# Kernel optimization log

Hardware: AMD Instinct MI355X
Metric: run time of the kernel (lower is better)

## Reference

```python
import jax, jax.numpy as jnp
import numpy as np

B, H, W, C = 8, 112, 112, 128
NH, WS, SR, HIDDEN = 4, 7, 8, 512
EPS = 1e-5

def ln(x, g, b):
    mu = jnp.mean(x, axis=-1, keepdims=True)
    var = jnp.var(x, axis=-1, keepdims=True)
    return (x - mu) * jax.lax.rsqrt(var + EPS) * g + b

def local_attn(x, qkv_w, qkv_b, pw, pb):
    # windowed attention: (H,W) tiled into WSxWS windows, H%WS==W%WS==0 so no pad
    Bx, N, Cx = x.shape
    hd = Cx // NH
    _h, _w = H // WS, W // WS
    xw = x.reshape(Bx, _h, WS, _w, WS, Cx).transpose(0, 1, 3, 2, 4, 5)
    xw = xw.reshape(Bx, _h * _w, WS * WS, Cx)
    qkv = (xw @ qkv_w + qkv_b).reshape(Bx, _h * _w, WS * WS, 3, NH, hd)
    qkv = qkv.transpose(3, 0, 1, 4, 2, 5)  # 3, B, nW, NH, ws2, hd
    q, k, v = qkv[0], qkv[1], qkv[2]
    attn = jax.nn.softmax((q @ jnp.swapaxes(k, -2, -1)) * (hd ** -0.5), axis=-1)
    o = (attn @ v).transpose(0, 1, 3, 2, 4).reshape(Bx, _h, _w, WS, WS, Cx)
    o = o.transpose(0, 1, 3, 2, 4, 5).reshape(Bx, N, Cx)
    return o @ pw + pb

def global_attn(x, qw, qb, kvw, kvb, srw, srb, sng, snb, pw, pb):
    Bx, N, Cx = x.shape
    hd = Cx // NH
    q = (x @ qw + qb).reshape(Bx, N, NH, hd).transpose(0, 2, 1, 3)  # B,NH,N,hd
    xi = x.reshape(Bx, H, W, Cx)
    xs = jax.lax.conv_general_dilated(xi, srw, (SR, SR), 'VALID',
                                      dimension_numbers=('NHWC', 'HWIO', 'NHWC')) + srb
    xs = ln(xs.reshape(Bx, -1, Cx), sng, snb)  # B, M, C  (M = (H/SR)*(W/SR))
    kv = (xs @ kvw + kvb).reshape(Bx, -1, 2, NH, hd)
    k = kv[:, :, 0].transpose(0, 2, 1, 3)
    v = kv[:, :, 1].transpose(0, 2, 1, 3)
    attn = jax.nn.softmax(jnp.einsum('bhnd,bhmd->bhnm', q, k) * (hd ** -0.5), axis=-1)
    o = jnp.einsum('bhnm,bhmd->bhnd', attn, v).transpose(0, 2, 1, 3).reshape(Bx, N, Cx)
    return o @ pw + pb

def mlp(x, f1w, f1b, dww, dwb, f2w, f2b):
    h = x @ f1w + f1b
    hi = h.reshape(x.shape[0], H, W, HIDDEN)
    hi = jax.lax.conv_general_dilated(hi, dww, (1, 1), 'SAME',
                                      dimension_numbers=('NHWC', 'HWIO', 'NHWC'),
                                      feature_group_count=HIDDEN) + dwb
    h = jax.nn.gelu(hi.reshape(x.shape[0], -1, HIDDEN), approximate=False)
    return h @ f2w + f2b

def reference(x, l_n1_g, l_n1_b, l_qkv_w, l_qkv_b, l_pw, l_pb, l_n2_g, l_n2_b,
              l_f1w, l_f1b, l_dww, l_dwb, l_f2w, l_f2b,
              g_n1_g, g_n1_b, g_qw, g_qb, g_kvw, g_kvb, g_srw, g_srb, g_sng, g_snb,
              g_pw, g_pb, g_n2_g, g_n2_b, g_f1w, g_f1b, g_dww, g_dwb, g_f2w, g_f2b):
    # Local-attention Block
    x = x + local_attn(ln(x, l_n1_g, l_n1_b), l_qkv_w, l_qkv_b, l_pw, l_pb)
    x = x + mlp(ln(x, l_n2_g, l_n2_b), l_f1w, l_f1b, l_dww, l_dwb, l_f2w, l_f2b)
    # Global (spatial-reduction) attention Block
    x = x + global_attn(ln(x, g_n1_g, g_n1_b), g_qw, g_qb, g_kvw, g_kvb,
                        g_srw, g_srb, g_sng, g_snb, g_pw, g_pb)
    x = x + mlp(ln(x, g_n2_g, g_n2_b), g_f1w, g_f1b, g_dww, g_dwb, g_f2w, g_f2b)
    return x

def setup_inputs() -> dict:
    key = jax.random.key(0)
    cnt = [0]
    def rn(shp, s=0.02):
        cnt[0] += 1
        return (jax.random.normal(jax.random.fold_in(key, cnt[0]), shp, dtype=jnp.float32) * s)
    z = lambda shp: jnp.zeros(shp, jnp.float32)
    o = lambda shp: jnp.ones(shp, jnp.float32)
    return {
        'x': rn((B, H * W, C), 1.0),
        'l_n1_g': o((C,)), 'l_n1_b': z((C,)),
        'l_qkv_w': rn((C, 3 * C)), 'l_qkv_b': z((3 * C,)),
        'l_pw': rn((C, C)), 'l_pb': z((C,)),
        'l_n2_g': o((C,)), 'l_n2_b': z((C,)),
        'l_f1w': rn((C, HIDDEN)), 'l_f1b': z((HIDDEN,)),
        'l_dww': rn((3, 3, 1, HIDDEN), 0.1), 'l_dwb': z((HIDDEN,)),
        'l_f2w': rn((HIDDEN, C)), 'l_f2b': z((C,)),
        'g_n1_g': o((C,)), 'g_n1_b': z((C,)),
        'g_qw': rn((C, C)), 'g_qb': z((C,)),
        'g_kvw': rn((C, 2 * C)), 'g_kvb': z((2 * C,)),
        'g_srw': rn((SR, SR, C, C), 0.02), 'g_srb': z((C,)),
        'g_sng': o((C,)), 'g_snb': z((C,)),
        'g_pw': rn((C, C)), 'g_pb': z((C,)),
        'g_n2_g': o((C,)), 'g_n2_b': z((C,)),
        'g_f1w': rn((C, HIDDEN)), 'g_f1b': z((HIDDEN,)),
        'g_dww': rn((3, 3, 1, HIDDEN), 0.1), 'g_dwb': z((HIDDEN,)),
        'g_f2w': rn((HIDDEN, C)), 'g_f2b': z((C,)),
    }
```

## Files before the change

### kernel.cpp

```cpp
#include <hip/hip_runtime.h>
#include <hip/hip_bf16.h>

#define DI __device__ __forceinline__

typedef __attribute__((ext_vector_type(8))) __bf16 bf16x8;
typedef __attribute__((ext_vector_type(8))) short short8;
typedef __attribute__((ext_vector_type(4))) short short4v;
typedef __attribute__((ext_vector_type(4))) float f32x4;

DI short f2b(float f) {
    union { float f; unsigned u; } v; v.f = f;
    unsigned r = v.u + 0x7FFFu + ((v.u >> 16) & 1u);
    return (short)(r >> 16);
}
DI float b2f(short s) {
    union { unsigned u; float f; } v; v.u = ((unsigned)(unsigned short)s) << 16;
    return v.f;
}
DI float lo16(int x) {
    union { unsigned u; float f; } v; v.u = (unsigned)x << 16; return v.f;
}
DI float hi16(int x) {
    union { unsigned u; float f; } v; v.u = (unsigned)x & 0xffff0000u; return v.f;
}

DI void gll16(const short* g, short* l) {
    __builtin_amdgcn_global_load_lds(
        (const __attribute__((address_space(1))) void*)(g),
        (__attribute__((address_space(3))) void*)(l), 16, 0, 0);
}

DI float gelu(float a) {
    float z = fabsf(a) * 0.7071067811865475f;
    float t = __builtin_amdgcn_rcpf(fmaf(0.3275911f, z, 1.f));
    float p = t * fmaf(t, fmaf(t, fmaf(t, fmaf(t, 1.061405429f, -1.453152027f),
                                       1.421413741f), -0.284496736f), 0.254829592f);
    float e = __expf(-z * z);
    float er = fmaf(-p, e, 1.f);
    float sg = (a >= 0.f) ? er : -er;
    return 0.5f * a * (1.f + sg);
}

template<int OB, int HB, int HR, int LNO>
__global__ __launch_bounds__(512)
void gemm128(const short* __restrict__ A, int lda,
             const short* __restrict__ Wt, int ldw,
             const float* __restrict__ bias,
             void* __restrict__ Cv, int ldc,
             const short* __restrict__ R, int ldr,
             const float* __restrict__ lng, const float* __restrict__ lnb,
             short* __restrict__ lnout,
             int K)
{
    __shared__ short As[8192];
    __shared__ short Bs[8192];
    const int nx = gridDim.x;
    const int total = nx * gridDim.y;
    int bid = blockIdx.x + nx * blockIdx.y;
    if ((total & 7) == 0) bid = (bid & 7) * (total >> 3) + (bid >> 3);
    const int m0 = (bid / nx) * 128, n0 = (bid % nx) * 128;
    const int tid = threadIdx.x, lane = tid & 63, w = tid >> 6;
    const int wr = w >> 2, wc = w & 3;
    const int fr = lane & 15, fg = lane >> 4;
    const int mB = wr * 64 + fr;
    const int nB = wc * 32 + fg * 4;

    const int r0 = tid >> 2, p0 = tid & 3;
    const int s0 = (r0 & 3) ^ ((r0 >> 2) & 3);
    const short* aptr0 = A + (long long)(m0 + r0) * lda + (p0 ^ s0) * 8;
    const short* bptr0 = Wt + (long long)(n0 + r0) * ldw + (p0 ^ s0) * 8;

    const int sf = (fr & 3) ^ ((fr >> 2) & 3);
    const short* pA = As + (wr * 64 + fr) * 32 + (fg ^ sf) * 8;
    const short* pB = Bs + (wc * 32 + fr) * 32 + (fg ^ sf) * 8;

    int2 rpre[4][2];
    if (HR) {
        #pragma unroll
        for (int mi = 0; mi < 4; mi++) {
            const long long m = m0 + mB + mi * 16;
            #pragma unroll
            for (int ni = 0; ni < 2; ni++)
                rpre[mi][ni] = *(const int2*)&R[m * ldr + n0 + nB + ni * 16];
        }
    }

    f32x4 zero = {0.f, 0.f, 0.f, 0.f};
    f32x4 acc[4][2];
    #pragma unroll
    for (int i = 0; i < 4; i++)
        #pragma unroll
        for (int j = 0; j < 2; j++) acc[i][j] = zero;

    auto STAGE = [&](int buf, int t) {
        const int o = t * 32;
        gll16(aptr0 + o, As + buf * 4096 + w * 512);
        gll16(bptr0 + o, Bs + buf * 4096 + w * 512);
    };
    auto COMPUTE = [&](int buf) {
        const short* qA = pA + buf * 4096;
        const short* qB = pB + buf * 4096;
        bf16x8 af[4], bfr[2];
        #pragma unroll
        for (int i = 0; i < 4; i++) af[i] = *(const bf16x8*)(qA + i * 512);
        #pragma unroll
        for (int j = 0; j < 2; j++) bfr[j] = *(const bf16x8*)(qB + j * 512);
        __builtin_amdgcn_s_setprio(1);
        #pragma unroll
        for (int i = 0; i < 4; i++)
            #pragma unroll
            for (int j = 0; j < 2; j++)
                acc[i][j] = __builtin_amdgcn_mfma_f32_16x16x32_bf16(bfr[j], af[i], acc[i][j], 0, 0, 0);
        __builtin_amdgcn_s_setprio(0);
    };

    const int NT = K >> 5;
    STAGE(0, 0);
    for (int t = 0; t < NT; t++) {
        if (t + 1 < NT) {
            STAGE((t + 1) & 1, t + 1);
            asm volatile("s_waitcnt vmcnt(2)" ::: "memory");
        } else {
            asm volatile("s_waitcnt vmcnt(0)" ::: "memory");
        }
        __builtin_amdgcn_s_barrier();
        COMPUTE(t & 1);
        __builtin_amdgcn_s_barrier();
    }

    if (LNO) {
        float s1[4] = {0.f, 0.f, 0.f, 0.f}, s2[4] = {0.f, 0.f, 0.f, 0.f};
        #pragma unroll
        for (int mi = 0; mi < 4; mi++) {
            const long long m = m0 + mB + mi * 16;
            #pragma unroll
            for (int ni = 0; ni < 2; ni++) {
                const int n = nB + ni * 16;
                float4 bv = *(const float4*)&bias[n];
                const float* bvp = (const float*)&bv;
                float rv[4] = {lo16(rpre[mi][ni].x), hi16(rpre[mi][ni].x),
                               lo16(rpre[mi][ni].y), hi16(rpre[mi][ni].y)};
                #pragma unroll
                for (int v = 0; v < 4; v++) {
                    float val = acc[mi][ni][v] + bvp[v] + rv[v];
                    acc[mi][ni][v] = val;
                    s1[mi] += val;
                    s2[mi] += val * val;
                }
                int2 pk;
                pk.x = ((int)(unsigned short)f2b(acc[mi][ni][1]) << 16) | (unsigned short)f2b(acc[mi][ni][0]);
                pk.y = ((int)(unsigned short)f2b(acc[mi][ni][3]) << 16) | (unsigned short)f2b(acc[mi][ni][2]);
                *(int2*)&((short*)Cv)[m * ldc + n] = pk;
            }
        }
        #pragma unroll
        for (int mi = 0; mi < 4; mi++) {
            s1[mi] += __shfl_xor(s1[mi], 16); s1[mi] += __shfl_xor(s1[mi], 32);
            s2[mi] += __shfl_xor(s2[mi], 16); s2[mi] += __shfl_xor(s2[mi], 32);
        }
        float* sc = (float*)As;
        __syncthreads();
        if (fg == 0) {
            #pragma unroll
            for (int mi = 0; mi < 4; mi++) {
                int rt = mB + mi * 16;
                sc[rt * 8 + wc * 2]     = s1[mi];
                sc[rt * 8 + wc * 2 + 1] = s2[mi];
            }
        }
        __syncthreads();
        #pragma unroll
        for (int mi = 0; mi < 4; mi++) {
            int rt = mB + mi * 16;
            long long m = m0 + rt;
            float t1 = (sc[rt * 8 + 0] + sc[rt * 8 + 2]) + (sc[rt * 8 + 4] + sc[rt * 8 + 6]);
            float t2 = (sc[rt * 8 + 1] + sc[rt * 8 + 3]) + (sc[rt * 8 + 5] + sc[rt * 8 + 7]);
            float mu = t1 * 0.0078125f;
            float var = t2 * 0.0078125f - mu * mu;
            float rs = rsqrtf(var + 1e-5f);
            #pragma unroll
            for (int ni = 0; ni < 2; ni++) {
                int n = nB + ni * 16;
                float4 gg = *(const float4*)&lng[n];
                float4 bb = *(const float4*)&lnb[n];
                const float* gp = (const float*)&gg;
                const float* bp = (const float*)&bb;
                short o[4];
                #pragma unroll
                for (int v = 0; v < 4; v++)
                    o[v] = f2b((acc[mi][ni][v] - mu) * rs * gp[v] + bp[v]);
                int2 pk;
                pk.x = ((int)(unsigned short)o[1] << 16) | (unsigned short)o[0];
                pk.y = ((int)(unsigned short)o[3] << 16) | (unsigned short)o[2];
                *(int2*)&lnout[m * 128 + n] = pk;
            }
        }
    } else {
        #pragma unroll
        for (int mi = 0; mi < 4; mi++) {
            const long long m = m0 + mB + mi * 16;
            #pragma unroll
            for (int ni = 0; ni < 2; ni++) {
                const int n = n0 + nB + ni * 16;
                float4 bv = {0.f, 0.f, 0.f, 0.f};
                if (HB) bv = *(const float4*)&bias[n];
                const float* bvp = (const float*)&bv;
                float rv[4] = {0.f, 0.f, 0.f, 0.f};
                if (HR) {
                    rv[0] = lo16(rpre[mi][ni].x); rv[1] = hi16(rpre[mi][ni].x);
                    rv[2] = lo16(rpre[mi][ni].y); rv[3] = hi16(rpre[mi][ni].y);
                }
                float val[4];
                #pragma unroll
                for (int v = 0; v < 4; v++)
                    val[v] = acc[mi][ni][v] + bvp[v] + rv[v];
                if (OB) {
                    int2 pk;
                    pk.x = ((int)(unsigned short)f2b(val[1]) << 16) | (unsigned short)f2b(val[0]);
                    pk.y = ((int)(unsigned short)f2b(val[3]) << 16) | (unsigned short)f2b(val[2]);
                    *(int2*)&((short*)Cv)[m * ldc + n] = pk;
                } else {
                    float4 st = {val[0], val[1], val[2], val[3]};
                    *(float4*)&((float*)Cv)[m * ldc + n] = st;
                }
            }
        }
    }
}

template<int OB, int HB>
__global__ __launch_bounds__(256)
void gemm64(const short* __restrict__ A, int lda, long long sA,
            const short* __restrict__ Wt, int ldw, long long sW,
            const float* __restrict__ bias,
            void* __restrict__ Cv, int ldc, long long sC,
            int M, int N, int K)
{
    __shared__ short As[2048];
    __shared__ short Bs[2048];
    const int z = blockIdx.z;
    A  += (long long)z * sA;
    Wt += (long long)z * sW;
    const int m0 = blockIdx.y * 64, n0 = blockIdx.x * 64;
    const int tid = threadIdx.x, lane = tid & 63, wv = tid >> 6;
    const int wr = wv >> 1, wc = wv & 1;
    const int lrow = tid >> 2, lch = tid & 3;
    const int wch = lch ^ (lrow & 3);

    f32x4 zero = {0.f, 0.f, 0.f, 0.f};
    f32x4 acc00 = zero, acc01 = zero, acc10 = zero, acc11 = zero;

    const short* arow = &A[(long long)(m0 + lrow) * lda + lch * 8];
    const short* brow = &Wt[(long long)(n0 + lrow) * ldw + lch * 8];
    short* asw = &As[lrow * 32 + wch * 8];
    short* bsw = &Bs[lrow * 32 + wch * 8];

    const int fr = lane & 15, fg = lane >> 4;
    const int c = ((fg ^ (fr & 3)) * 8);
    const int a0off = (wr * 32 + fr) * 32 + c;
    const int b0off = (wc * 32 + fr) * 32 + c;

    for (int k0 = 0; k0 < K; k0 += 32) {
        uint4 av = *(const uint4*)arow; arow += 32;
        uint4 bv = *(const uint4*)brow; brow += 32;
        __syncthreads();
        *(uint4*)asw = av;
        *(uint4*)bsw = bv;
        __syncthreads();
        bf16x8 a0 = *(const bf16x8*)&As[a0off];
        bf16x8 a1 = *(const bf16x8*)&As[a0off + 512];
        bf16x8 b0 = *(const bf16x8*)&Bs[b0off];
        bf16x8 b1 = *(const bf16x8*)&Bs[b0off + 512];
        acc00 = __builtin_amdgcn_mfma_f32_16x16x32_bf16(a0, b0, acc00, 0, 0, 0);
        acc01 = __builtin_amdgcn_mfma_f32_16x16x32_bf16(a0, b1, acc01, 0, 0, 0);
        acc10 = __builtin_amdgcn_mfma_f32_16x16x32_bf16(a1, b0, acc10, 0, 0, 0);
        acc11 = __builtin_amdgcn_mfma_f32_16x16x32_bf16(a1, b1, acc11, 0, 0, 0);
    }

    const long long cz = (long long)z * sC;
    const int rbase = m0 + wr * 32 + fg * 4;
    const int cbase = n0 + wc * 32 + fr;
    auto emit = [&](f32x4 a, int mi, int ni) {
        int cc = cbase + ni * 16;
        if (cc >= N) return;
        float bv = HB ? bias[cc] : 0.f;
        #pragma unroll
        for (int v = 0; v < 4; v++) {
            int rr = rbase + mi * 16 + v;
            if (rr >= M) continue;
            float val = a[v] + bv;
            if (OB) ((short*)Cv)[cz + (long long)rr * ldc + cc] = f2b(val);
            else    ((float*)Cv)[cz + (long long)rr * ldc + cc] = val;
        }
    };
    emit(acc00, 0, 0); emit(acc01, 0, 1); emit(acc10, 1, 0); emit(acc11, 1, 1);
}

__global__ __launch_bounds__(256)
void srgemm(const short* __restrict__ LNF, const short* __restrict__ Wt,
            float* __restrict__ PART)
{
    __shared__ short As[2048];
    __shared__ short Bs[2048];
    const int z = blockIdx.z;
    const int m0 = blockIdx.y * 64, n0 = blockIdx.x * 64;
    const int tid = threadIdx.x, lane = tid & 63, wv = tid >> 6;
    const int wr = wv >> 1, wc = wv & 1;
    const int lrow = tid >> 2, lch = tid & 3;
    const int wch = lch ^ (lrow & 3);

    f32x4 zero = {0.f, 0.f, 0.f, 0.f};
    f32x4 acc00 = zero, acc01 = zero, acc10 = zero, acc11 = zero;

    int row = m0 + lrow;
    int rc = row < 1568 ? row : 1567;
    int b = rc / 196, p = rc % 196;
    int oh = p / 14, ow = p % 14;
    int k0 = z * 256;
    int kh = k0 >> 10, koff = k0 & 1023;
    const short* arow = LNF + ((long long)(b * 12544 + (oh * 8 + kh) * 112 + ow * 8)) * 128
                        + koff + lch * 8;
    const short* brow = Wt + (long long)(n0 + lrow) * 8192 + k0 + lch * 8;
    short* asw = &As[lrow * 32 + wch * 8];
    short* bsw = &Bs[lrow * 32 + wch * 8];

    const int fr = lane & 15, fg = lane >> 4;
    const int c = ((fg ^ (fr & 3)) * 8);
    const int a0off = (wr * 32 + fr) * 32 + c;
    const int b0off = (wc * 32 + fr) * 32 + c;

    for (int kk = 0; kk < 256; kk += 32) {
        uint4 av = *(const uint4*)arow; arow += 32;
        uint4 bv = *(const uint4*)brow; brow += 32;
        __syncthreads();
        *(uint4*)asw = av;
        *(uint4*)bsw = bv;
        __syncthreads();
        bf16x8 a0 = *(const bf16x8*)&As[a0off];
        bf16x8 a1 = *(const bf16x8*)&As[a0off + 512];
        bf16x8 b0 = *(const bf16x8*)&Bs[b0off];
        bf16x8 b1 = *(const bf16x8*)&Bs[b0off + 512];
        acc00 = __builtin_amdgcn_mfma_f32_16x16x32_bf16(a0, b0, acc00, 0, 0, 0);
        acc01 = __builtin_amdgcn_mfma_f32_16x16x32_bf16(a0, b1, acc01, 0, 0, 0);
        acc10 = __builtin_amdgcn_mfma_f32_16x16x32_bf16(a1, b0, acc10, 0, 0, 0);
        acc11 = __builtin_amdgcn_mfma_f32_16x16x32_bf16(a1, b1, acc11, 0, 0, 0);
    }

    const int rbase = m0 + wr * 32 + fg * 4;
    const int cbase = n0 + wc * 32 + fr;
    auto emit = [&](f32x4 a, int mi, int ni) {
        int cc = cbase + ni * 16;
        #pragma unroll
        for (int v = 0; v < 4; v++) {
            int rr = rbase + mi * 16 + v;
            if (rr >= 1568) continue;
            PART[(long long)z * 200704 + (long long)rr * 128 + cc] = a[v];
        }
    };
    emit(acc00, 0, 0); emit(acc01, 0, 1); emit(acc10, 1, 0); emit(acc11, 1, 1);
}

__global__ void reduceXS(const float* __restrict__ PART, const float* __restrict__ bias,
                         float* __restrict__ XS)
{
    int i = blockIdx.x * 256 + threadIdx.x;
    float s = 0.f;
    #pragma unroll
    for (int z = 0; z < 32; z++) s += PART[(long long)z * 200704 + i];
    XS[i] = s + bias[i & 127];
}

__global__ __launch_bounds__(256)
void ln_kernel(const float* __restrict__ x, const float* __restrict__ g,
               const float* __restrict__ b, short* __restrict__ o, int rows)
{
    int row = blockIdx.x * 4 + (threadIdx.x >> 6);
    if (row >= rows) return;
    int lane = threadIdx.x & 63;
    const float2 v = *(const float2*)&x[(long long)row * 128 + lane * 2];
    float s = v.x + v.y;
    float ss = v.x * v.x + v.y * v.y;
    #pragma unroll
    for (int off = 1; off < 64; off <<= 1) {
        s += __shfl_xor(s, off);
        ss += __shfl_xor(ss, off);
    }
    float mu = s * 0.0078125f;
    float var = ss * 0.0078125f - mu * mu;
    float rs = rsqrtf(var + 1e-5f);
    float2 gg = *(const float2*)&g[lane * 2];
    float2 bb = *(const float2*)&b[lane * 2];
    short2 out;
    out.x = f2b((v.x - mu) * rs * gg.x + bb.x);
    out.y = f2b((v.y - mu) * rs * gg.y + bb.y);
    *(short2*)&o[(long long)row * 128 + lane * 2] = out;
}

__global__ __launch_bounds__(256)
void ln_first(const float* __restrict__ x, const float* __restrict__ g,
              const float* __restrict__ b, short* __restrict__ o,
              short* __restrict__ res)
{
    int row = blockIdx.x * 4 + (threadIdx.x >> 6);
    int lane = threadIdx.x & 63;
    const float2 v = *(const float2*)&x[(long long)row * 128 + lane * 2];
    short2 rc;
    rc.x = f2b(v.x); rc.y = f2b(v.y);
    *(short2*)&res[(long long)row * 128 + lane * 2] = rc;
    float s = v.x + v.y;
    float ss = v.x * v.x + v.y * v.y;
    #pragma unroll
    for (int off = 1; off < 64; off <<= 1) {
        s += __shfl_xor(s, off);
        ss += __shfl_xor(ss, off);
    }
    float mu = s * 0.0078125f;
    float var = ss * 0.0078125f - mu * mu;
    float rs = rsqrtf(var + 1e-5f);
    float2 gg = *(const float2*)&g[lane * 2];
    float2 bb = *(const float2*)&b[lane * 2];
    short2 out;
    out.x = f2b((v.x - mu) * rs * gg.x + bb.x);
    out.y = f2b((v.y - mu) * rs * gg.y + bb.y);
    *(short2*)&o[(long long)row * 128 + lane * 2] = out;
}

__global__ void wtrans(const float* __restrict__ w, short* __restrict__ wt, int K, int N)
{
    long long idx = (long long)blockIdx.x * 256 + threadIdx.x;
    if (idx >= (long long)K * N) return;
    int k = (int)(idx / N), n = (int)(idx % N);
    wt[(long long)n * K + k] = f2b(w[idx]);
}

__global__ void packkv(const short* __restrict__ kvb, short* __restrict__ kp,
                       short* __restrict__ vt)
{
    int idx = blockIdx.x * 256 + threadIdx.x;
    if (idx >= 229376) return;
    int d = idx & 31;
    int m = (idx >> 5) % 224;
    int bh = idx / (224 * 32);
    int b = bh >> 2, h = bh & 3;
    short kv = 0, vv = 0;
    if (m < 196) {
        long long src = ((long long)b * 196 + m) * 256 + h * 32 + d;
        kv = kvb[src];
        vv = kvb[src + 128];
    }
    if (m < 208) kp[((long long)bh * 208 + m) * 32 + d] = kv;
    vt[((long long)bh * 32 + d) * 224 + m] = vv;
}

__global__ __launch_bounds__(512)
void lattn(const short* __restrict__ qkv, short* __restrict__ att)
{
    __shared__ short QKs[64 * 264];
    __shared__ short Vt[128 * 72];
    __shared__ short Pl[8 * 16 * 72];
    const int bi = blockIdx.x >> 8;
    const int win = blockIdx.x & 255;
    const int wy = win >> 4, wx = win & 15;
    const long long base = (long long)bi * 12544;
    const int tid = threadIdx.x;

    for (int i = tid; i < 1152; i += 512) {
        uint4 zz = {0, 0, 0, 0};
        *(uint4*)&Vt[i * 8] = zz;
    }
    __syncthreads();

    for (int idx = tid; idx < 2352; idx += 512) {
        int i = idx / 48, ch = idx % 48;
        long long n = base + (wy * 7 + i / 7) * 112 + wx * 7 + i % 7;
        uint4 v = *(const uint4*)&qkv[n * 384 + ch * 8];
        if (ch < 32) {
            *(uint4*)&QKs[i * 264 + ch * 8] = v;
        } else {
            int c0 = (ch - 32) * 8;
            const short* sp = (const short*)&v;
            #pragma unroll
            for (int u = 0; u < 8; u++) {
                int cc = c0 + u;
                Vt[cc * 72 + ((((i >> 3) ^ ((cc >> 3) & 7)) << 3) | (i & 7))] = sp[u];
            }
        }
    }
    __syncthreads();

    const int w = tid >> 6, l = tid & 63;
    const int h = w >> 1, qh = w & 1;
    const int q16 = l & 15, g = l >> 4;
    const float SC = 0.17677669529663689f;
    f32x4 zero = {0.f, 0.f, 0.f, 0.f};

    bf16x8 kf[4];
    #pragma unroll
    for (int kt = 0; kt < 4; kt++)
        kf[kt] = *(const bf16x8*)&QKs[(kt * 16 + q16) * 264 + 128 + h * 32 + g * 8];
    bf16x8 vf[2][2];
    #pragma unroll
    for (int dt = 0; dt < 2; dt++) {
        int cc = h * 32 + dt * 16 + q16;
        #pragma unroll
        for (int s2 = 0; s2 < 2; s2++)
            vf[dt][s2] = *(const bf16x8*)&Vt[cc * 72 + (((s2 * 4 + g) ^ ((cc >> 3) & 7)) << 3)];
    }
    short* pw = &Pl[(w * 16 + q16) * 72];

    for (int qt2 = 0; qt2 < 2; qt2++) {
        int qt = qh * 2 + qt2;
        bf16x8 qf = *(const bf16x8*)&QKs[(qt * 16 + q16) * 264 + h * 32 + g * 8];
        f32x4 s[4];
        #pragma unroll
        for (int kt = 0; kt < 4; kt++)
            s[kt] = __builtin_amdgcn_mfma_f32_16x16x32_bf16(kf[kt], qf, zero, 0, 0, 0);
        float mx = -1e30f;
        #pragma unroll
        for (int kt = 0; kt < 4; kt++) {
            #pragma unroll
            for (int v = 0; v < 4; v++) {
                int k = kt * 16 + g * 4 + v;
                if (k < 49) mx = fmaxf(mx, s[kt][v]);
            }
        }
        mx = fmaxf(mx, __shfl_xor(mx, 16));
        mx = fmaxf(mx, __shfl_xor(mx, 32));
        float sum = 0.f;
        #pragma unroll
        for (int kt = 0; kt < 4; kt++) {
            #pragma unroll
            for (int v = 0; v < 4; v++) {
                int k = kt * 16 + g * 4 + v;
                float p = (k < 49) ? __expf(SC * (s[kt][v] - mx)) : 0.f;
                s[kt][v] = p;
                sum += p;
            }
        }
        sum += __shfl_xor(sum, 16);
        sum += __shfl_xor(sum, 32);
        float inv = 1.f / sum;
        #pragma unroll
        for (int kt = 0; kt < 4; kt++) {
            int lo = ((int)(unsigned short)f2b(s[kt][1] * inv) << 16) | (unsigned short)f2b(s[kt][0] * inv);
            int hi = ((int)(unsigned short)f2b(s[kt][3] * inv) << 16) | (unsigned short)f2b(s[kt][2] * inv);
            int2 pr; pr.x = lo; pr.y = hi;
            *(int2*)&pw[kt * 16 + g * 4] = pr;
        }
        f32x4 o0 = zero, o1 = zero;
        #pragma unroll
        for (int s2 = 0; s2 < 2; s2++) {
            bf16x8 pa = *(const bf16x8*)&pw[s2 * 32 + g * 8];
            o0 = __builtin_amdgcn_mfma_f32_16x16x32_bf16(pa, vf[0][s2], o0, 0, 0, 0);
            o1 = __builtin_amdgcn_mfma_f32_16x16x32_bf16(pa, vf[1][s2], o1, 0, 0, 0);
        }
        #pragma unroll
        for (int v = 0; v < 4; v++) {
            int q = qt * 16 + g * 4 + v;
            if (q < 49) {
                long long n = base + (wy * 7 + q / 7) * 112 + wx * 7 + q % 7;
                att[n * 128 + h * 32 + q16]      = f2b(o0[v]);
                att[n * 128 + h * 32 + 16 + q16] = f2b(o1[v]);
            }
        }
    }
}

__global__ __launch_bounds__(256)
void gattn(const short* __restrict__ Q, const short* __restrict__ KP,
           const short* __restrict__ VT, short* __restrict__ O)
{
    __shared__ short Ks[208 * 40];
    __shared__ short Vt[32 * 232];
    __shared__ short Pl[4 * 16 * 232];
    const int qb = blockIdx.x;
    const int bh = blockIdx.y;
    const int b = bh >> 2, h = bh & 3;
    const int tid = threadIdx.x, w = tid >> 6, l = tid & 63;
    const int q16 = l & 15, g = l >> 4;

    for (int idx = tid; idx < 832; idx += 256) {
        int m = idx >> 2, dg = idx & 3;
        uint4 v = *(const uint4*)&KP[((long long)bh * 208 + m) * 32 + dg * 8];
        *(uint4*)&Ks[m * 40 + ((dg ^ (m & 3)) * 8)] = v;
    }
    for (int idx = tid; idx < 896; idx += 256) {
        int d = idx / 28, mg = idx % 28;
        uint4 v = *(const uint4*)&VT[((long long)bh * 32 + d) * 224 + mg * 8];
        *(uint4*)&Vt[d * 232 + mg * 8] = v;
    }
    const long long qbase = (long long)b * 12544 + qb * 128 + w * 32;
    bf16x8 qfa = *(const bf16x8*)&Q[(qbase + q16) * 128 + h * 32 + g * 8];
    bf16x8 qfb = *(const bf16x8*)&Q[(qbase + 16 + q16) * 128 + h * 32 + g * 8];
    __syncthreads();

    const float SC = 0.17677669529663689f;
    f32x4 zero = {0.f, 0.f, 0.f, 0.f};
    short* pw = &Pl[(w * 16 + q16) * 232];
    const int xk = (g ^ (q16 & 3)) * 8;

    #pragma unroll
    for (int qt = 0; qt < 2; qt++) {
        bf16x8 qf = qt ? qfb : qfa;
        f32x4 s[13];
        #pragma unroll
        for (int t = 0; t < 13; t++) {
            bf16x8 a = *(const bf16x8*)&Ks[(t * 16 + q16) * 40 + xk];
            s[t] = __builtin_amdgcn_mfma_f32_16x16x32_bf16(a, qf, zero, 0, 0, 0);
        }
        float mx = -1e30f;
        #pragma unroll
        for (int t = 0; t < 13; t++) {
            #pragma unroll
            for (int v = 0; v < 4; v++) {
                int k = t * 16 + g * 4 + v;
                if (k < 196) mx = fmaxf(mx, s[t][v]);
            }
        }
        mx = fmaxf(mx, __shfl_xor(mx, 16));
        mx = fmaxf(mx, __shfl_xor(mx, 32));
        float sum = 0.f;
        #pragma unroll
        for (int t = 0; t < 13; t++) {
            #pragma unroll
            for (int v = 0; v < 4; v++) {
                int k = t * 16 + g * 4 + v;
                float pv = (k < 196) ? __expf(SC * (s[t][v] - mx)) : 0.f;
                s[t][v] = pv;
                sum += pv;
            }
        }
        sum += __shfl_xor(sum, 16);
        sum += __shfl_xor(sum, 32);
        float inv = 1.f / sum;
        #pragma unroll
        for (int t = 0; t < 13; t++) {
            int lo = ((int)(unsigned short)f2b(s[t][1] * inv) << 16) | (unsigned short)f2b(s[t][0] * inv);
            int hi = ((int)(unsigned short)f2b(s[t][3] * inv) << 16) | (unsigned short)f2b(s[t][2] * inv);
            int2 pr; pr.x = lo; pr.y = hi;
            *(int2*)&pw[t * 16 + g * 4] = pr;
        }
        int2 zz; zz.x = 0; zz.y = 0;
        *(int2*)&pw[208 + g * 4] = zz;

        f32x4 o0 = zero, o1 = zero;
        #pragma unroll
        for (int kc = 0; kc < 7; kc++) {
            bf16x8 pa = *(const bf16x8*)&pw[kc * 32 + g * 8];
            bf16x8 v0 = *(const bf16x8*)&Vt[q16 * 232 + kc * 32 + g * 8];
            bf16x8 v1 = *(const bf16x8*)&Vt[(16 + q16) * 232 + kc * 32 + g * 8];
            o0 = __builtin_amdgcn_mfma_f32_16x16x32_bf16(v0, pa, o0, 0, 0, 0);
            o1 = __builtin_amdgcn_mfma_f32_16x16x32_bf16(v1, pa, o1, 0, 0, 0);
        }
        const long long r = qbase + qt * 16 + q16;
        int2 p0, p1;
        p0.x = ((int)(unsigned short)f2b(o0[1]) << 16) | (unsigned short)f2b(o0[0]);
        p0.y = ((int)(unsigned short)f2b(o0[3]) << 16) | (unsigned short)f2b(o0[2]);
        p1.x = ((int)(unsigned short)f2b(o1[1]) << 16) | (unsigned short)f2b(o1[0]);
        p1.y = ((int)(unsigned short)f2b(o1[3]) << 16) | (unsigned short)f2b(o1[2]);
        *(int2*)&O[r * 128 + h * 32 + g * 4]      = p0;
        *(int2*)&O[r * 128 + h * 32 + 16 + g * 4] = p1;
    }
}

__global__ __launch_bounds__(256)
void dwgelu(const short* __restrict__ h1, const float* __restrict__ w,
            const float* __restrict__ bias, short* __restrict__ h2)
{
    int bid = blockIdx.x;
    bid = (bid & 7) * (gridDim.x >> 3) + (bid >> 3);
    const int idx = bid * 256 + threadIdx.x;
    const int cg = idx & 127;
    const int rem = idx >> 7;
    const int img = rem / 1568;
    const int t = rem % 1568;
    const int x0 = (t % 56) * 2;
    const int y0 = (t / 56) * 4;
    const int c0 = cg << 2;

    float wreg[9][4];
    #pragma unroll
    for (int tp = 0; tp < 9; tp++) {
        float4 v = *(const float4*)&w[tp * 512 + c0];
        wreg[tp][0] = v.x; wreg[tp][1] = v.y; wreg[tp][2] = v.z; wreg[tp][3] = v.w;
    }
    float4 bv = *(const float4*)&bias[c0];
    float acc[4][2][4];
    #pragma unroll
    for (int r = 0; r < 4; r++)
        #pragma unroll
        for (int oc = 0; oc < 2; oc++) {
            acc[r][oc][0] = bv.x; acc[r][oc][1] = bv.y;
            acc[r][oc][2] = bv.z; acc[r][oc][3] = bv.w;
        }
    const long long ibase = (long long)img * 12544;

    if (x0 >= 1 && x0 <= 109 && y0 >= 1 && y0 <= 107) {
        const short* base = &h1[(ibase + (long long)(y0 - 1) * 112 + (x0 - 1)) * 512 + c0];
        #pragma unroll
        for (int dy = 0; dy < 6; dy++) {
            float rowf[4][4];
            #pragma unroll
            for (int kx = 0; kx < 4; kx++) {
                short4v sv = *(const short4v*)&base[((long long)dy * 112 + kx) * 512];
                #pragma unroll
                for (int u = 0; u < 4; u++) rowf[kx][u] = b2f(sv[u]);
            }
            #pragma unroll
            for (int ky = 0; ky < 3; ky++) {
                const int r = dy - ky;
                if (r < 0 || r > 3) continue;
                #pragma unroll
                for (int oc = 0; oc < 2; oc++)
                    #pragma unroll
                    for (int kx = 0; kx < 3; kx++)
                        #pragma unroll
                        for (int u = 0; u < 4; u++)
                            acc[r][oc][u] = fmaf(rowf[oc + kx][u], wreg[ky * 3 + kx][u], acc[r][oc][u]);
            }
        }
    } else {
        #pragma unroll
        for (int dy = -1; dy <= 4; dy++) {
            const int yy = y0 + dy;
            const bool rowok = (unsigned)yy < 112u;
            float rowf[4][4];
            #pragma unroll
            for (int kx = 0; kx < 4; kx++) {
                const int xx = x0 - 1 + kx;
                short4v sv = {0, 0, 0, 0};
                if (rowok && (unsigned)xx < 112u)
                    sv = *(const short4v*)&h1[(ibase + yy * 112 + xx) * 512 + c0];
                #pragma unroll
                for (int u = 0; u < 4; u++) rowf[kx][u] = b2f(sv[u]);
            }
            #pragma unroll
            for (int ky = 0; ky < 3; ky++) {
                const int r = dy + 1 - ky;
                if (r < 0 || r > 3) continue;
                #pragma unroll
                for (int oc = 0; oc < 2; oc++)
                    #pragma unroll
                    for (int kx = 0; kx < 3; kx++)
                        #pragma unroll
                        for (int u = 0; u < 4; u++)
                            acc[r][oc][u] = fmaf(rowf[oc + kx][u], wreg[ky * 3 + kx][u], acc[r][oc][u]);
            }
        }
    }
    #pragma unroll
    for (int r = 0; r < 4; r++)
        #pragma unroll
        for (int oc = 0; oc < 2; oc++) {
            short o[4];
            #pragma unroll
            for (int u = 0; u < 4; u++) o[u] = f2b(gelu(acc[r][oc][u]));
            int2 pk;
            pk.x = ((int)(unsigned short)o[1] << 16) | (unsigned short)o[0];
            pk.y = ((int)(unsigned short)o[3] << 16) | (unsigned short)o[2];
            *(int2*)&h2[(ibase + (y0 + r) * 112 + x0 + oc) * 512 + c0] = pk;
        }
}

extern "C" void kernel_launch(void* const* d_in, const int* in_sizes, int n_in,
                              void* d_out, int out_size, void* d_ws, size_t ws_size,
                              hipStream_t stream)
{
    (void)in_sizes; (void)n_in; (void)out_size;
    const float* X      = (const float*)d_in[0];
    const float* l_n1_g = (const float*)d_in[1];
    const float* l_n1_b = (const float*)d_in[2];
    const float* l_qkv_w= (const float*)d_in[3];
    const float* l_qkv_b= (const float*)d_in[4];
    const float* l_pw   = (const float*)d_in[5];
    const float* l_pb   = (const float*)d_in[6];
    const float* l_n2_g = (const float*)d_in[7];
    const float* l_n2_b = (const float*)d_in[8];
    const float* l_f1w  = (const float*)d_in[9];
    const float* l_f1b  = (const float*)d_in[10];
    const float* l_dww  = (const float*)d_in[11];
    const float* l_dwb  = (const float*)d_in[12];
    const float* l_f2w  = (const float*)d_in[13];
    const float* l_f2b  = (const float*)d_in[14];
    const float* g_n1_g = (const float*)d_in[15];
    const float* g_n1_b = (const float*)d_in[16];
    const float* g_qw   = (const float*)d_in[17];
    const float* g_qb   = (const float*)d_in[18];
    const float* g_kvw  = (const float*)d_in[19];
    const float* g_kvb  = (const float*)d_in[20];
    const float* g_srw  = (const float*)d_in[21];
    const float* g_srb  = (const float*)d_in[22];
    const float* g_sng  = (const float*)d_in[23];
    const float* g_snb  = (const float*)d_in[24];
    const float* g_pw   = (const float*)d_in[25];
    const float* g_pb   = (const float*)d_in[26];
    const float* g_n2_g = (const float*)d_in[27];
    const float* g_n2_b = (const float*)d_in[28];
    const float* g_f1w  = (const float*)d_in[29];
    const float* g_f1b  = (const float*)d_in[30];
    const float* g_dww  = (const float*)d_in[31];
    const float* g_dwb  = (const float*)d_in[32];
    const float* g_f2w  = (const float*)d_in[33];
    const float* g_f2b  = (const float*)d_in[34];

    const long long NPB = 12544;
    const long long BN  = 100352;
    const int iBN = (int)BN;

    float* OUT = (float*)d_out;
    char* ws = (char*)d_ws;
    size_t off = 0;
    auto alloc = [&](size_t bytes) { size_t o = off; off += (bytes + 255) & ~(size_t)255; return o; };
    short* WT_QKV = (short*)(ws + alloc(384 * 128 * 2));
    short* WT_LPW = (short*)(ws + alloc(128 * 128 * 2));
    short* WT_LF1 = (short*)(ws + alloc(512 * 128 * 2));
    short* WT_LF2 = (short*)(ws + alloc(128 * 512 * 2));
    short* WT_GQ  = (short*)(ws + alloc(128 * 128 * 2));
    short* WT_GKV = (short*)(ws + alloc(256 * 128 * 2));
    short* WT_GSR = (short*)(ws + alloc(128 * 8192 * 2));
    short* WT_GPW = (short*)(ws + alloc(128 * 128 * 2));
    short* WT_GF1 = (short*)(ws + alloc(512 * 128 * 2));
    short* WT_GF2 = (short*)(ws + alloc(128 * 512 * 2));
    short* LNF    = (short*)(ws + alloc((size_t)BN * 128 * 2));
    short* RES    = (short*)(ws + alloc((size_t)BN * 128 * 2));
    char*  U      = ws + alloc(0);

    const size_t SZ_H1   = (size_t)BN * 512 * 2;
    const bool big = ws_size >= off + 2 * SZ_H1 + 4096;
    short* QKVB = (short*)(U + 0);
    short* ATT  = (short*)(U + 77070336);
    float* PART = (float*)(U + 0);
    float* XS   = (float*)(U + 25690368);
    short* XSLN = (short*)(U + 26493184);
    short* KVB  = (short*)(U + 26894592);
    short* QBUF = (short*)(U + 27697408);
    short* KP   = (short*)(U + 53387776);
    short* VT   = (short*)(U + 53387776 + 425984);

    wtrans<<<192, 256, 0, stream>>>(l_qkv_w, WT_QKV, 128, 384);
    wtrans<<<64, 256, 0, stream>>>(l_pw, WT_LPW, 128, 128);
    wtrans<<<256, 256, 0, stream>>>(l_f1w, WT_LF1, 128, 512);
    wtrans<<<256, 256, 0, stream>>>(l_f2w, WT_LF2, 512, 128);
    wtrans<<<64, 256, 0, stream>>>(g_qw, WT_GQ, 128, 128);
    wtrans<<<128, 256, 0, stream>>>(g_kvw, WT_GKV, 128, 256);
    wtrans<<<4096, 256, 0, stream>>>(g_srw, WT_GSR, 8192, 128);
    wtrans<<<64, 256, 0, stream>>>(g_pw, WT_GPW, 128, 128);
    wtrans<<<256, 256, 0, stream>>>(g_f1w, WT_GF1, 128, 512);
    wtrans<<<256, 256, 0, stream>>>(g_f2w, WT_GF2, 512, 128);

    const int CB = big ? 8 : 2;
    short* H1 = (short*)(U + 0);

    ln_first<<<25088, 256, 0, stream>>>(X, l_n1_g, l_n1_b, LNF, RES);
    gemm128<1, 1, 0, 0><<<dim3(3, 784), 512, 0, stream>>>(
        LNF, 128, WT_QKV, 128, l_qkv_b, QKVB, 384, nullptr, 0,
        nullptr, nullptr, nullptr, 128);
    lattn<<<2048, 512, 0, stream>>>(QKVB, ATT);
    gemm128<1, 1, 1, 1><<<dim3(1, 784), 512, 0, stream>>>(
        ATT, 128, WT_LPW, 128, l_pb, RES, 128, RES, 128,
        l_n2_g, l_n2_b, LNF, 128);

    {
        short* H2 = (short*)(U + (size_t)CB * NPB * 512 * 2);
        for (int b0 = 0; b0 < 8; b0 += CB) {
            int Mc = CB * 12544;
            gemm128<1, 1, 0, 0><<<dim3(4, Mc / 128), 512, 0, stream>>>(
                LNF + (long long)b0 * NPB * 128, 128, WT_LF1, 128, l_f1b,
                H1, 512, nullptr, 0, nullptr, nullptr, nullptr, 128);
            dwgelu<<<CB * 784, 256, 0, stream>>>(H1, l_dww, l_dwb, H2);
            gemm128<1, 1, 1, 1><<<dim3(1, Mc / 128), 512, 0, stream>>>(
                H2, 512, WT_LF2, 512, l_f2b,
                RES + (long long)b0 * NPB * 128, 128,
                RES + (long long)b0 * NPB * 128, 128,
                g_n1_g, g_n1_b, LNF + (long long)b0 * NPB * 128, 512);
        }
    }

    gemm128<1, 1, 0, 0><<<dim3(1, 784), 512, 0, stream>>>(
        LNF, 128, WT_GQ, 128, g_qb, QBUF, 128, nullptr, 0,
        nullptr, nullptr, nullptr, 128);
    srgemm<<<dim3(2, 25, 32), 256, 0, stream>>>(LNF, WT_GSR, PART);
    reduceXS<<<784, 256, 0, stream>>>(PART, g_srb, XS);
    ln_kernel<<<392, 256, 0, stream>>>(XS, g_sng, g_snb, XSLN, 1568);
    gemm64<1, 1><<<dim3(4, 25, 1), 256, 0, stream>>>(
        XSLN, 128, 0, WT_GKV, 128, 0, g_kvb,
        KVB, 256, 0, 1568, 256, 128);
    packkv<<<896, 256, 0, stream>>>(KVB, KP, VT);
    gattn<<<dim3(98, 32), 256, 0, stream>>>(QBUF, KP, VT, ATT);
    gemm128<1, 1, 1, 1><<<dim3(1, 784), 512, 0, stream>>>(
        ATT, 128, WT_GPW, 128, g_pb, RES, 128, RES, 128,
        g_n2_g, g_n2_b, LNF, 128);

    {
        short* H2 = (short*)(U + (size_t)CB * NPB * 512 * 2);
        for (int b0 = 0; b0 < 8; b0 += CB) {
            int Mc = CB * 12544;
            gemm128<1, 1, 0, 0><<<dim3(4, Mc / 128), 512, 0, stream>>>(
                LNF + (long long)b0 * NPB * 128, 128, WT_GF1, 128, g_f1b,
                H1, 512, nullptr, 0, nullptr, nullptr, nullptr, 128);
            dwgelu<<<CB * 784, 256, 0, stream>>>(H1, g_dww, g_dwb, H2);
            gemm128<0, 1, 1, 0><<<dim3(1, Mc / 128), 512, 0, stream>>>(
                H2, 512, WT_GF2, 512, g_f2b,
                OUT + (long long)b0 * NPB * 128, 128,
                RES + (long long)b0 * NPB * 128, 128,
                nullptr, nullptr, nullptr, 512);
        }
    }
}
```

Baseline: 564.7 us.

## Load full K=128 tile in one shot and widen K step to 64 in GEMM

Adds a FULLK path to gemm128 for the K=128 GEMMs. It stages the whole 128x128 A and B tiles into LDS with a single wait and barrier, then runs four MFMA k-steps with an XOR-swizzled layout, removing the per-32 pipeline barriers. The K=512 GEMMs keep the double-buffered loop but move to 64-wide K stages with a new swizzle, halving the number of barrier iterations. LDS use doubles to 64 KB per block, which may lower occupancy, and the FULLK path gives up overlap between loads and compute.

```diff
diff --git a/kernel.cpp b/kernel.cpp
--- a/kernel.cpp
+++ b/kernel.cpp
@@ -41,7 +41,7 @@
     return 0.5f * a * (1.f + sg);
 }
 
-template<int OB, int HB, int HR, int LNO>
+template<int OB, int HB, int HR, int LNO, int FULLK>
 __global__ __launch_bounds__(512)
 void gemm128(const short* __restrict__ A, int lda,
              const short* __restrict__ Wt, int ldw,
@@ -52,8 +52,8 @@
              short* __restrict__ lnout,
              int K)
 {
-    __shared__ short As[8192];
-    __shared__ short Bs[8192];
+    __shared__ short As[16384];
+    __shared__ short Bs[16384];
     const int nx = gridDim.x;
     const int total = nx * gridDim.y;
     int bid = blockIdx.x + nx * blockIdx.y;
@@ -64,15 +64,7 @@
     const int fr = lane & 15, fg = lane >> 4;
     const int mB = wr * 64 + fr;
     const int nB = wc * 32 + fg * 4;
-
-    const int r0 = tid >> 2, p0 = tid & 3;
-    const int s0 = (r0 & 3) ^ ((r0 >> 2) & 3);
-    const short* aptr0 = A + (long long)(m0 + r0) * lda + (p0 ^ s0) * 8;
-    const short* bptr0 = Wt + (long long)(n0 + r0) * ldw + (p0 ^ s0) * 8;
-
-    const int sf = (fr & 3) ^ ((fr >> 2) & 3);
-    const short* pA = As + (wr * 64 + fr) * 32 + (fg ^ sf) * 8;
-    const short* pB = Bs + (wc * 32 + fr) * 32 + (fg ^ sf) * 8;
+    const int x7 = fr & 7;
 
     int2 rpre[4][2];
     if (HR) {
@@ -92,40 +84,83 @@
         #pragma unroll
         for (int j = 0; j < 2; j++) acc[i][j] = zero;
 
-    auto STAGE = [&](int buf, int t) {
-        const int o = t * 32;
-        gll16(aptr0 + o, As + buf * 4096 + w * 512);
-        gll16(bptr0 + o, Bs + buf * 4096 + w * 512);
-    };
-    auto COMPUTE = [&](int buf) {
-        const short* qA = pA + buf * 4096;
-        const short* qB = pB + buf * 4096;
-        bf16x8 af[4], bfr[2];
-        #pragma unroll
-        for (int i = 0; i < 4; i++) af[i] = *(const bf16x8*)(qA + i * 512);
-        #pragma unroll
-        for (int j = 0; j < 2; j++) bfr[j] = *(const bf16x8*)(qB + j * 512);
+    if (FULLK) {
+        #pragma unroll
+        for (int i = 0; i < 4; i++) {
+            const int row = i * 32 + w * 4 + (lane >> 4);
+            const int chunk = lane & 15;
+            const int scol = (chunk ^ (row & 7)) * 8;
+            short* dA = As + (i * 32 + w * 4) * 128 + lane * 8;
+            short* dB = Bs + (i * 32 + w * 4) * 128 + lane * 8;
+            gll16(A  + (long long)(m0 + row) * lda + scol, dA);
+            gll16(Wt + (long long)(n0 + row) * ldw + scol, dB);
+        }
+        asm volatile("s_waitcnt vmcnt(0)" ::: "memory");
+        __builtin_amdgcn_s_barrier();
         __builtin_amdgcn_s_setprio(1);
         #pragma unroll
-        for (int i = 0; i < 4; i++)
-            #pragma unroll
-            for (int j = 0; j < 2; j++)
-                acc[i][j] = __builtin_amdgcn_mfma_f32_16x16x32_bf16(bfr[j], af[i], acc[i][j], 0, 0, 0);
+        for (int kt = 0; kt < 4; kt++) {
+            const int kc = ((kt * 4 + fg) ^ x7) * 8;
+            bf16x8 af[4], bfr[2];
+            #pragma unroll
+            for (int mi = 0; mi < 4; mi++)
+                af[mi] = *(const bf16x8*)(As + (mB + mi * 16) * 128 + kc);
+            #pragma unroll
+            for (int ni = 0; ni < 2; ni++)
+                bfr[ni] = *(const bf16x8*)(Bs + (wc * 32 + ni * 16 + fr) * 128 + kc);
+            #pragma unroll
+            for (int mi = 0; mi < 4; mi++)
+                #pragma unroll
+                for (int ni = 0; ni < 2; ni++)
+                    acc[mi][ni] = __builtin_amdgcn_mfma_f32_16x16x32_bf16(bfr[ni], af[mi], acc[mi][ni], 0, 0, 0);
+        }
         __builtin_amdgcn_s_setprio(0);
-    };
-
-    const int NT = K >> 5;
-    STAGE(0, 0);
-    for (int t = 0; t < NT; t++) {
-        if (t + 1 < NT) {
-            STAGE((t + 1) & 1, t + 1);
-            asm volatile("s_waitcnt vmcnt(2)" ::: "memory");
-        } else {
-            asm volatile("s_waitcnt vmcnt(0)" ::: "memory");
-        }
-        __builtin_amdgcn_s_barrier();
-        COMPUTE(t & 1);
-        __builtin_amdgcn_s_barrier();
+    } else {
+        auto STAGE = [&](int buf, int t) {
+            #pragma unroll
+            for (int i = 0; i < 2; i++) {
+                const int row = i * 64 + w * 8 + (lane >> 3);
+                const int chunk = lane & 7;
+                const int scol = t * 64 + (chunk ^ (row & 7)) * 8;
+                short* dA = As + buf * 8192 + (i * 64 + w * 8) * 64 + lane * 8;
+                short* dB = Bs + buf * 8192 + (i * 64 + w * 8) * 64 + lane * 8;
+                gll16(A  + (long long)(m0 + row) * lda + scol, dA);
+                gll16(Wt + (long long)(n0 + row) * ldw + scol, dB);
+            }
+        };
+        auto COMPUTE = [&](int buf) {
+            __builtin_amdgcn_s_setprio(1);
+            #pragma unroll
+            for (int kt = 0; kt < 2; kt++) {
+                const int kc = ((kt * 4 + fg) ^ x7) * 8;
+                bf16x8 af[4], bfr[2];
+                #pragma unroll
+                for (int mi = 0; mi < 4; mi++)
+                    af[mi] = *(const bf16x8*)(As + buf * 8192 + (mB + mi * 16) * 64 + kc);
+                #pragma unroll
+                for (int ni = 0; ni < 2; ni++)
+                    bfr[ni] = *(const bf16x8*)(Bs + buf * 8192 + (wc * 32 + ni * 16 + fr) * 64 + kc);
+                #pragma unroll
+                for (int mi = 0; mi < 4; mi++)
+                    #pragma unroll
+                    for (int ni = 0; ni < 2; ni++)
+                        acc[mi][ni] = __builtin_amdgcn_mfma_f32_16x16x32_bf16(bfr[ni], af[mi], acc[mi][ni], 0, 0, 0);
+            }
+            __builtin_amdgcn_s_setprio(0);
+        };
+        const int NT = K >> 6;
+        STAGE(0, 0);
+        for (int t = 0; t < NT; t++) {
+            if (t + 1 < NT) {
+                STAGE((t + 1) & 1, t + 1);
+                asm volatile("s_waitcnt vmcnt(4)" ::: "memory");
+            } else {
+                asm volatile("s_waitcnt vmcnt(0)" ::: "memory");
+            }
+            __builtin_amdgcn_s_barrier();
+            COMPUTE(t & 1);
+            __builtin_amdgcn_s_barrier();
+        }
     }
 
     if (LNO) {
@@ -852,11 +887,11 @@
     short* H1 = (short*)(U + 0);
 
     ln_first<<<25088, 256, 0, stream>>>(X, l_n1_g, l_n1_b, LNF, RES);
-    gemm128<1, 1, 0, 0><<<dim3(3, 784), 512, 0, stream>>>(
+    gemm128<1, 1, 0, 0, 1><<<dim3(3, 784), 512, 0, stream>>>(
         LNF, 128, WT_QKV, 128, l_qkv_b, QKVB, 384, nullptr, 0,
         nullptr, nullptr, nullptr, 128);
     lattn<<<2048, 512, 0, stream>>>(QKVB, ATT);
-    gemm128<1, 1, 1, 1><<<dim3(1, 784), 512, 0, stream>>>(
+    gemm128<1, 1, 1, 1, 1><<<dim3(1, 784), 512, 0, stream>>>(
         ATT, 128, WT_LPW, 128, l_pb, RES, 128, RES, 128,
         l_n2_g, l_n2_b, LNF, 128);
 
@@ -864,11 +899,11 @@
         short* H2 = (short*)(U + (size_t)CB * NPB * 512 * 2);
         for (int b0 = 0; b0 < 8; b0 += CB) {
             int Mc = CB * 12544;
-            gemm128<1, 1, 0, 0><<<dim3(4, Mc / 128), 512, 0, stream>>>(
+            gemm128<1, 1, 0, 0, 1><<<dim3(4, Mc / 128), 512, 0, stream>>>(
                 LNF + (long long)b0 * NPB * 128, 128, WT_LF1, 128, l_f1b,
                 H1, 512, nullptr, 0, nullptr, nullptr, nullptr, 128);
             dwgelu<<<CB * 784, 256, 0, stream>>>(H1, l_dww, l_dwb, H2);
-            gemm128<1, 1, 1, 1><<<dim3(1, Mc / 128), 512, 0, stream>>>(
+            gemm128<1, 1, 1, 1, 0><<<dim3(1, Mc / 128), 512, 0, stream>>>(
                 H2, 512, WT_LF2, 512, l_f2b,
                 RES + (long long)b0 * NPB * 128, 128,
                 RES + (long long)b0 * NPB * 128, 128,
@@ -876,7 +911,7 @@
         }
     }
 
-    gemm128<1, 1, 0, 0><<<dim3(1, 784), 512, 0, stream>>>(
+    gemm128<1, 1, 0, 0, 1><<<dim3(1, 784), 512, 0, stream>>>(
         LNF, 128, WT_GQ, 128, g_qb, QBUF, 128, nullptr, 0,
         nullptr, nullptr, nullptr, 128);
     srgemm<<<dim3(2, 25, 32), 256, 0, stream>>>(LNF, WT_GSR, PART);
@@ -887,7 +922,7 @@
         KVB, 256, 0, 1568, 256, 128);
     packkv<<<896, 256, 0, stream>>>(KVB, KP, VT);
     gattn<<<dim3(98, 32), 256, 0, stream>>>(QBUF, KP, VT, ATT);
-    gemm128<1, 1, 1, 1><<<dim3(1, 784), 512, 0, stream>>>(
+    gemm128<1, 1, 1, 1, 1><<<dim3(1, 784), 512, 0, stream>>>(
         ATT, 128, WT_GPW, 128, g_pb, RES, 128, RES, 128,
         g_n2_g, g_n2_b, LNF, 128);
 
@@ -895,11 +930,11 @@
         short* H2 = (short*)(U + (size_t)CB * NPB * 512 * 2);
         for (int b0 = 0; b0 < 8; b0 += CB) {
             int Mc = CB * 12544;
-            gemm128<1, 1, 0, 0><<<dim3(4, Mc / 128), 512, 0, stream>>>(
+            gemm128<1, 1, 0, 0, 1><<<dim3(4, Mc / 128), 512, 0, stream>>>(
                 LNF + (long long)b0 * NPB * 128, 128, WT_GF1, 128, g_f1b,
                 H1, 512, nullptr, 0, nullptr, nullptr, nullptr, 128);
             dwgelu<<<CB * 784, 256, 0, stream>>>(H1, g_dww, g_dwb, H2);
-            gemm128<0, 1, 1, 0><<<dim3(1, Mc / 128), 512, 0, stream>>>(
+            gemm128<0, 1, 1, 0, 0><<<dim3(1, Mc / 128), 512, 0, stream>>>(
                 H2, 512, WT_GF2, 512, g_f2b,
                 OUT + (long long)b0 * NPB * 128, 128,
                 RES + (long long)b0 * NPB * 128, 128,
```

Measured after the change: 558.0 us. About the same (-1.2%).
